# Optimization experiments

Measured on AMD Instinct MI355X. Metric: run time of the kernel, lower is better.

Reference implementation:

```python
import jax, jax.numpy as jnp
import numpy as np

T, H = 8192, 2048


def setup_inputs() -> dict:
    key = jax.random.key(0)
    k1, k2, k3 = jax.random.split(key, 3)
    x_sequence = jax.random.normal(k1, (T, H), dtype=jnp.float32)
    lamda = jax.random.normal(k2, (H,), dtype=jnp.float32) * 0.2
    B = jax.random.normal(k3, (H, H), dtype=jnp.float32) / np.sqrt(H).astype(np.float32)
    return {"x_sequence": x_sequence, "lamda": lamda, "B": B}


def reference(x_sequence, lamda, B):
    # Batched input projection: u_t = B @ x_t for all t -> one GEMM. [T, H]
    u = x_sequence @ B.T
    # Linear diagonal recurrence h_t = lamda * h_{t-1} + u_t with h_0 = 0,
    # solved with a log-depth associative scan over (a, b) pairs where
    # combine((a1,b1),(a2,b2)) = (a2*a1, a2*b1 + b2).
    a = jnp.broadcast_to(lamda, u.shape)  # [T, H]

    def combine(c1, c2):
        a1, b1 = c1
        a2, b2 = c2
        return (a2 * a1, a2 * b1 + b2)

    _, h = jax.lax.associative_scan(combine, (a, u))
    return h  # [T, H] stacked hidden states
```

## Files before the change

kernel.cpp:

```cpp
#include <hip/hip_runtime.h>
#include <hip/hip_bf16.h>


#define TDIM 8192
#define HDIM 2048
#define BM 256
#define BN 256
#define BK 32
#define NT (HDIM / BK)
#define ASLOT 8192
#define BSLOT 8192
#define LCH 64
#define GCH (TDIM / LCH)

#define XBF_BYTES (TDIM * HDIM * 2)
#define BBF_BYTES (HDIM * HDIM * 2)
#define E_BYTES   (GCH * HDIM * 4)
#define WS_NEED   ((size_t)XBF_BYTES + BBF_BYTES + E_BYTES)

typedef float f32x4 __attribute__((ext_vector_type(4)));
typedef short s16x4 __attribute__((ext_vector_type(4)));
typedef short s16x8 __attribute__((ext_vector_type(8)));

static __device__ __forceinline__ short f2bf(float f) {
  __bf16 b = (__bf16)f;
  return __builtin_bit_cast(short, b);
}

#define SB()   asm volatile("s_barrier" ::: "memory")
#define VMW(n) asm volatile("s_waitcnt vmcnt(" #n ")" ::: "memory")
#define GL(gp, lp)                                                            \
  __builtin_amdgcn_global_load_lds(                                           \
      (const __attribute__((address_space(1))) void*)(gp),                    \
      (__attribute__((address_space(3))) void*)(lp), 16, 0, 0)

__global__ void cvt_fast2(const float* __restrict__ X, const float* __restrict__ Bm,
                          short* __restrict__ Xb, short* __restrict__ Bb) {
  const int b = blockIdx.x;
  const float* s;
  short* d;
  int base;
  if (b < 4096) { s = X;  d = Xb; base = b * 1024; }
  else          { s = Bm; d = Bb; base = (b - 4096) * 1024; }
  const int t = threadIdx.x;
  f32x4 v0 = *(const f32x4*)(s + (size_t)(base +   0 + t) * 4);
  f32x4 v1 = *(const f32x4*)(s + (size_t)(base + 256 + t) * 4);
  f32x4 v2 = *(const f32x4*)(s + (size_t)(base + 512 + t) * 4);
  f32x4 v3 = *(const f32x4*)(s + (size_t)(base + 768 + t) * 4);
#define STORE1(v_, off_) do {                                                 \
    s16x4 o;                                                                  \
    o[0] = f2bf(v_[0]); o[1] = f2bf(v_[1]);                                   \
    o[2] = f2bf(v_[2]); o[3] = f2bf(v_[3]);                                   \
    *(s16x4*)(d + (size_t)(base + (off_) + t) * 4) = o;                       \
  } while (0)
  STORE1(v0, 0);
  STORE1(v1, 256);
  STORE1(v2, 512);
  STORE1(v3, 768);
#undef STORE1
}

__global__ __launch_bounds__(512, 2) void gemm8p2(
    const short* __restrict__ Xb, const short* __restrict__ Bb,
    float* __restrict__ U) {
  extern __shared__ __align__(16) short smem[];
  short* As = smem;
  short* Bs = smem + 4 * ASLOT;

  const int wg  = blockIdx.x;
  const int swz = (wg & 7) * 32 + (wg >> 3);
  const int tm = swz >> 3;
  const int tn = swz & 7;
  const int row0 = tm * BM, col0 = tn * BN;

  const int tid  = threadIdx.x;
  const int lane = tid & 63;
  const int wid  = tid >> 6;
  const int wr = (wid >> 2) * 128;
  const int wc = (wid & 3) * 64;
  const int r16 = lane & 15;
  const int ks8 = (lane >> 4) * 8;

  int offA[8], offB[4];
#pragma unroll
  for (int m = 0; m < 8; ++m) {
    const int r = wr + m * 16 + r16;
    offA[m] = r * BK + (ks8 ^ (((r >> 1) & 3) * 8));
  }
#pragma unroll
  for (int n = 0; n < 4; ++n) {
    const int r = wc + n * 16 + r16;
    offB[n] = r * BK + (ks8 ^ (((r >> 1) & 3) * 8));
  }

  const int srow = tid >> 2;
  const int sg   = (tid & 3) ^ ((tid >> 3) & 3);
  const short* gA0 = Xb + (size_t)(row0 + srow) * HDIM + sg * 8;
  const short* gA1 = gA0 + (size_t)128 * HDIM;
  const short* gB0 = Bb + (size_t)(col0 + srow) * HDIM + sg * 8;
  const short* gB1 = gB0 + (size_t)128 * HDIM;

  f32x4 acc[8][4] = {};

#pragma unroll
  for (int k = 0; k < 3; ++k) {
    GL(gA0 + k * BK, &As[k * ASLOT + tid * 8]);
    GL(gA1 + k * BK, &As[k * ASLOT + 4096 + tid * 8]);
    GL(gB0 + k * BK, &Bs[k * BSLOT + tid * 8]);
    GL(gB1 + k * BK, &Bs[k * BSLOT + 4096 + tid * 8]);
  }
  VMW(8);
  SB();

#define ITER(J_, ST_, VMA_, SBF_) do {                                        \
    const int sc_ = (J_) & 3;                                                 \
    const int si_ = ((J_) + 3) & 3;                                           \
    const int ko_ = ((J_) + 3) * BK;                                          \
    s16x8 af[4], bfv[4];                                                      \
    _Pragma("unroll") for (int m = 0; m < 4; ++m)                             \
      af[m] = *(const s16x8*)&As[sc_ * ASLOT + offA[m]];                      \
    _Pragma("unroll") for (int n = 0; n < 4; ++n)                             \
      bfv[n] = *(const s16x8*)&Bs[sc_ * BSLOT + offB[n]];                     \
    if (ST_) {                                                                \
      GL(gA0 + ko_, &As[si_ * ASLOT + tid * 8]);                              \
      GL(gA1 + ko_, &As[si_ * ASLOT + 4096 + tid * 8]);                       \
    }                                                                         \
    SB();                                                                     \
    __builtin_amdgcn_s_setprio(1);                                            \
    _Pragma("unroll") for (int m = 0; m < 4; ++m)                             \
      _Pragma("unroll") for (int n = 0; n < 4; ++n)                           \
        acc[m][n] = __builtin_amdgcn_mfma_f32_16x16x32_bf16(                  \
            af[m], bfv[n], acc[m][n], 0, 0, 0);                               \
    __builtin_amdgcn_s_setprio(0);                                            \
    SB();                                                                     \
    _Pragma("unroll") for (int m = 0; m < 4; ++m)                             \
      af[m] = *(const s16x8*)&As[sc_ * ASLOT + offA[4 + m]];                  \
    if (ST_) {                                                                \
      GL(gB0 + ko_, &Bs[si_ * BSLOT + tid * 8]);                              \
      GL(gB1 + ko_, &Bs[si_ * BSLOT + 4096 + tid * 8]);                       \
    }                                                                         \
    SB();                                                                     \
    __builtin_amdgcn_s_setprio(1);                                            \
    _Pragma("unroll") for (int m = 0; m < 4; ++m)                             \
      _Pragma("unroll") for (int n = 0; n < 4; ++n)                           \
        acc[4 + m][n] = __builtin_amdgcn_mfma_f32_16x16x32_bf16(              \
            af[m], bfv[n], acc[4 + m][n], 0, 0, 0);                           \
    __builtin_amdgcn_s_setprio(0);                                            \
    VMA_;                                                                     \
    SBF_;                                                                     \
  } while (0)

#pragma unroll 4
  for (int j = 0; j < NT - 4; ++j) ITER(j, true, VMW(8), SB());
  ITER(NT - 4, true,  VMW(8), SB());
  ITER(NT - 3, false, VMW(4), SB());
  ITER(NT - 2, false, VMW(0), SB());
  ITER(NT - 1, false, (void)0, (void)0);
#undef ITER

  const int crow = row0 + wr + ((lane >> 4) << 2);
  const int ccol = col0 + wc + r16;
#pragma unroll
  for (int m = 0; m < 8; ++m)
#pragma unroll
    for (int n = 0; n < 4; ++n)
#pragma unroll
      for (int j = 0; j < 4; ++j)
        U[(size_t)(crow + m * 16 + j) * HDIM + ccol + n * 16] = acc[m][n][j];
}

__global__ __launch_bounds__(256, 2) void gemm_f32_fb(
    const float* __restrict__ X, const float* __restrict__ Bm,
    float* __restrict__ U) {
#define LDK 40
#define FBM 128
#define FBK 32
#define FNT (HDIM / FBK)
  __shared__ __align__(16) short As[2][FBM * LDK];
  __shared__ __align__(16) short Bs[2][FBM * LDK];
  const int wg  = blockIdx.x;
  const int cpx = (TDIM / FBM) * (HDIM / FBM) / 8;
  const int swz = (wg & 7) * cpx + (wg >> 3);
  const int tm = swz >> 4;
  const int tn = swz & 15;
  const int row0 = tm * FBM, col0 = tn * FBM;
  const int tid  = threadIdx.x;
  const int lane = tid & 63;
  const int wid  = tid >> 6;
  const int wr = (wid >> 1) * 64;
  const int wc = (wid & 1) * 64;
  const int srow = tid >> 2;
  const int sk   = (tid & 3) << 3;
  const float* gA  = X  + (size_t)(row0 + srow) * HDIM + sk;
  const float* gA2 = gA + 64 * HDIM;
  const float* gB  = Bm + (size_t)(col0 + srow) * HDIM + sk;
  const float* gB2 = gB + 64 * HDIM;
  f32x4 a00, a01, a10, a11, b00, b01, b10, b11;
#define LOADREG(kt) do {                                                      \
    const float* p;                                                           \
    p = gA  + (kt) * FBK; a00 = *(const f32x4*)p; a01 = *(const f32x4*)(p+4); \
    p = gA2 + (kt) * FBK; a10 = *(const f32x4*)p; a11 = *(const f32x4*)(p+4); \
    p = gB  + (kt) * FBK; b00 = *(const f32x4*)p; b01 = *(const f32x4*)(p+4); \
    p = gB2 + (kt) * FBK; b10 = *(const f32x4*)p; b11 = *(const f32x4*)(p+4); \
  } while (0)
#define CVT8(v, lo, hi) do {                                                  \
    v[0] = f2bf(lo[0]); v[1] = f2bf(lo[1]); v[2] = f2bf(lo[2]);               \
    v[3] = f2bf(lo[3]); v[4] = f2bf(hi[0]); v[5] = f2bf(hi[1]);               \
    v[6] = f2bf(hi[2]); v[7] = f2bf(hi[3]);                                   \
  } while (0)
#define DSWRITE(buf) do {                                                     \
    s16x8 v;                                                                  \
    CVT8(v, a00, a01); *(s16x8*)&As[buf][srow * LDK + sk] = v;                \
    CVT8(v, a10, a11); *(s16x8*)&As[buf][(srow + 64) * LDK + sk] = v;         \
    CVT8(v, b00, b01); *(s16x8*)&Bs[buf][srow * LDK + sk] = v;                \
    CVT8(v, b10, b11); *(s16x8*)&Bs[buf][(srow + 64) * LDK + sk] = v;         \
  } while (0)
  f32x4 acc[4][4] = {};
#define COMPUTE(buf) do {                                                     \
    const int r16_ = lane & 15;                                               \
    const int ks_  = (lane >> 4) * 8;                                         \
    s16x8 af[4], bfr[4];                                                      \
    _Pragma("unroll") for (int m = 0; m < 4; ++m)                             \
      af[m] = *(const s16x8*)&As[buf][(wr + m * 16 + r16_) * LDK + ks_];      \
    _Pragma("unroll") for (int n = 0; n < 4; ++n)                             \
      bfr[n] = *(const s16x8*)&Bs[buf][(wc + n * 16 + r16_) * LDK + ks_];     \
    _Pragma("unroll") for (int m = 0; m < 4; ++m)                             \
      _Pragma("unroll") for (int n = 0; n < 4; ++n)                           \
        acc[m][n] = __builtin_amdgcn_mfma_f32_16x16x32_bf16(                  \
            af[m], bfr[n], acc[m][n], 0, 0, 0);                               \
  } while (0)
  LOADREG(0);
  DSWRITE(0);
  __syncthreads();
#pragma unroll 2
  for (int kt = 0; kt < FNT; ++kt) {
    const int cur = kt & 1;
    if (kt + 1 < FNT) LOADREG(kt + 1);
    COMPUTE(cur);
    if (kt + 1 < FNT) DSWRITE(cur ^ 1);
    __syncthreads();
  }
  const int crow = wr + ((lane >> 4) << 2);
  const int ccol = wc + (lane & 15);
#pragma unroll
  for (int m = 0; m < 4; ++m)
#pragma unroll
    for (int n = 0; n < 4; ++n)
#pragma unroll
      for (int j = 0; j < 4; ++j)
        U[(size_t)(row0 + crow + m * 16 + j) * HDIM + (col0 + ccol + n * 16)] =
            acc[m][n][j];
#undef LOADREG
#undef CVT8
#undef DSWRITE
#undef COMPUTE
#undef LDK
#undef FBM
#undef FBK
#undef FNT
}

__global__ void scan_pass1(const float* __restrict__ U,
                           const float* __restrict__ lam,
                           float* __restrict__ e) {
  const int c = (blockIdx.y * 256 + threadIdx.x) * 4;
  const int j = blockIdx.x;
  const f32x4 l4 = *(const f32x4*)&lam[c];
  f32x4 h = {0.f, 0.f, 0.f, 0.f};
  const float* up = U + (size_t)j * LCH * HDIM + c;
#pragma unroll 4
  for (int t = 0; t < LCH; ++t) {
    f32x4 u4 = *(const f32x4*)up;
    h = l4 * h + u4;
    up += HDIM;
  }
  *(f32x4*)&e[(size_t)j * HDIM + c] = h;
}

__global__ void scan_carry(float* __restrict__ e, const float* __restrict__ lam) {
  const int c = (blockIdx.x * 256 + threadIdx.x) * 4;
  const f32x4 l4 = *(const f32x4*)&lam[c];
  f32x4 p = l4;
#pragma unroll
  for (int i = 0; i < 6; ++i) p = p * p;
  f32x4 E = {0.f, 0.f, 0.f, 0.f};
  for (int j = 0; j < GCH; ++j) {
    f32x4 ej = *(const f32x4*)&e[(size_t)j * HDIM + c];
    *(f32x4*)&e[(size_t)j * HDIM + c] = E;
    E = p * E + ej;
  }
}

__global__ void scan_pass3(float* __restrict__ U, const float* __restrict__ lam,
                           const float* __restrict__ carry) {
  const int c = (blockIdx.y * 256 + threadIdx.x) * 4;
  const int j = blockIdx.x;
  const f32x4 l4 = *(const f32x4*)&lam[c];
  f32x4 h = *(const f32x4*)&carry[(size_t)j * HDIM + c];
  float* up = U + (size_t)j * LCH * HDIM + c;
#pragma unroll 4
  for (int t = 0; t < LCH; ++t) {
    f32x4 u4 = *(const f32x4*)up;
    h = l4 * h + u4;
    *(f32x4*)up = h;
    up += HDIM;
  }
}

extern "C" void kernel_launch(void* const* d_in, const int* in_sizes, int n_in,
                              void* d_out, int out_size, void* d_ws, size_t ws_size,
                              hipStream_t stream) {
  const float* X   = (const float*)d_in[0];
  const float* lam = (const float*)d_in[1];
  const float* Bm  = (const float*)d_in[2];
  float* U = (float*)d_out;

  if (ws_size >= WS_NEED) {
    short* Xb = (short*)d_ws;
    short* Bb = (short*)((char*)d_ws + XBF_BYTES);
    float* e  = (float*)((char*)d_ws + XBF_BYTES + BBF_BYTES);

    hipFuncSetAttribute((const void*)gemm8p2,
                        hipFuncAttributeMaxDynamicSharedMemorySize, 131072);

    cvt_fast2<<<dim3(5120), dim3(256), 0, stream>>>(X, Bm, Xb, Bb);
    gemm8p2<<<dim3((TDIM / BM) * (HDIM / BN)), dim3(512), 131072, stream>>>(
        Xb, Bb, U);
    scan_pass1<<<dim3(GCH, HDIM / 1024), dim3(256), 0, stream>>>(U, lam, e);
    scan_carry<<<dim3(HDIM / 1024), dim3(256), 0, stream>>>(e, lam);
    scan_pass3<<<dim3(GCH, HDIM / 1024), dim3(256), 0, stream>>>(U, lam, e);
  } else {
    float* e = (float*)d_ws;
    gemm_f32_fb<<<dim3((TDIM / 128) * (HDIM / 128)), dim3(256), 0, stream>>>(
        X, Bm, U);
    scan_pass1<<<dim3(GCH, HDIM / 1024), dim3(256), 0, stream>>>(U, lam, e);
    scan_carry<<<dim3(HDIM / 1024), dim3(256), 0, stream>>>(e, lam);
    scan_pass3<<<dim3(GCH, HDIM / 1024), dim3(256), 0, stream>>>(U, lam, e);
  }
}
```

Before: 128.8 us.

## Fuse X fp32-to-bf16 conversion into GEMM A-tile LDS read path

Drops the separate conversion pass over X. The GEMM now streams fp32 X tiles straight into LDS, using a new 4-byte XOR swizzle, and converts to bf16 when it reads the A fragments. The pipeline goes from 4 stages to 3 to fit the larger fp32 A tiles in LDS. This saves writing and rereading a 32 MB bf16 copy of X, but it doubles the global and LDS bytes for A and adds conversion ALU work inside the main loop.

```diff
diff --git a/kernel.cpp b/kernel.cpp
--- a/kernel.cpp
+++ b/kernel.cpp
@@ -8,15 +8,15 @@
 #define BN 256
 #define BK 32
 #define NT (HDIM / BK)
-#define ASLOT 8192
-#define BSLOT 8192
+#define AF 8192
+#define BS 8192
 #define LCH 64
 #define GCH (TDIM / LCH)
 
-#define XBF_BYTES (TDIM * HDIM * 2)
 #define BBF_BYTES (HDIM * HDIM * 2)
 #define E_BYTES   (GCH * HDIM * 4)
-#define WS_NEED   ((size_t)XBF_BYTES + BBF_BYTES + E_BYTES)
+#define WS_NEED   ((size_t)BBF_BYTES + E_BYTES)
+#define LDS_BYTES (3 * AF * 4 + 3 * BS * 2)
 
 typedef float f32x4 __attribute__((ext_vector_type(4)));
 typedef short s16x4 __attribute__((ext_vector_type(4)));
@@ -34,38 +34,30 @@
       (const __attribute__((address_space(1))) void*)(gp),                    \
       (__attribute__((address_space(3))) void*)(lp), 16, 0, 0)
 
-__global__ void cvt_fast2(const float* __restrict__ X, const float* __restrict__ Bm,
-                          short* __restrict__ Xb, short* __restrict__ Bb) {
+__global__ void cvt_B(const float* __restrict__ src, short* __restrict__ dst) {
   const int b = blockIdx.x;
-  const float* s;
-  short* d;
-  int base;
-  if (b < 4096) { s = X;  d = Xb; base = b * 1024; }
-  else          { s = Bm; d = Bb; base = (b - 4096) * 1024; }
+  const int base = b * 1024;
   const int t = threadIdx.x;
-  f32x4 v0 = *(const f32x4*)(s + (size_t)(base +   0 + t) * 4);
-  f32x4 v1 = *(const f32x4*)(s + (size_t)(base + 256 + t) * 4);
-  f32x4 v2 = *(const f32x4*)(s + (size_t)(base + 512 + t) * 4);
-  f32x4 v3 = *(const f32x4*)(s + (size_t)(base + 768 + t) * 4);
+  f32x4 v0 = *(const f32x4*)(src + (size_t)(base +   0 + t) * 4);
+  f32x4 v1 = *(const f32x4*)(src + (size_t)(base + 256 + t) * 4);
+  f32x4 v2 = *(const f32x4*)(src + (size_t)(base + 512 + t) * 4);
+  f32x4 v3 = *(const f32x4*)(src + (size_t)(base + 768 + t) * 4);
 #define STORE1(v_, off_) do {                                                 \
     s16x4 o;                                                                  \
     o[0] = f2bf(v_[0]); o[1] = f2bf(v_[1]);                                   \
     o[2] = f2bf(v_[2]); o[3] = f2bf(v_[3]);                                   \
-    *(s16x4*)(d + (size_t)(base + (off_) + t) * 4) = o;                       \
-  } while (0)
-  STORE1(v0, 0);
-  STORE1(v1, 256);
-  STORE1(v2, 512);
-  STORE1(v3, 768);
+    *(s16x4*)(dst + (size_t)(base + (off_) + t) * 4) = o;                     \
+  } while (0)
+  STORE1(v0, 0); STORE1(v1, 256); STORE1(v2, 512); STORE1(v3, 768);
 #undef STORE1
 }
 
-__global__ __launch_bounds__(512, 2) void gemm8p2(
-    const short* __restrict__ Xb, const short* __restrict__ Bb,
+__global__ __launch_bounds__(512, 2) void gemm_f32a(
+    const float* __restrict__ X, const short* __restrict__ Bb,
     float* __restrict__ U) {
-  extern __shared__ __align__(16) short smem[];
-  short* As = smem;
-  short* Bs = smem + 4 * ASLOT;
+  extern __shared__ __align__(16) char smemc[];
+  float* As = (float*)smemc;
+  short* Bs = (short*)(smemc + 3 * AF * 4);
 
   const int wg  = blockIdx.x;
   const int swz = (wg & 7) * 32 + (wg >> 3);
@@ -79,52 +71,56 @@
   const int wr = (wid >> 2) * 128;
   const int wc = (wid & 3) * 64;
   const int r16 = lane & 15;
-  const int ks8 = (lane >> 4) * 8;
+  const int g4  = lane >> 4;
+  const int ks8 = g4 * 8;
 
   int offA[8], offB[4];
 #pragma unroll
   for (int m = 0; m < 8; ++m) {
     const int r = wr + m * 16 + r16;
-    offA[m] = r * BK + (ks8 ^ (((r >> 1) & 3) * 8));
+    offA[m] = r * 32 + (((g4 * 2) ^ (r & 7)) << 2);
   }
 #pragma unroll
   for (int n = 0; n < 4; ++n) {
     const int r = wc + n * 16 + r16;
-    offB[n] = r * BK + (ks8 ^ (((r >> 1) & 3) * 8));
-  }
-
-  const int srow = tid >> 2;
-  const int sg   = (tid & 3) ^ ((tid >> 3) & 3);
-  const short* gA0 = Xb + (size_t)(row0 + srow) * HDIM + sg * 8;
-  const short* gA1 = gA0 + (size_t)128 * HDIM;
-  const short* gB0 = Bb + (size_t)(col0 + srow) * HDIM + sg * 8;
+    offB[n] = r * 32 + (ks8 ^ (((r >> 1) & 3) * 8));
+  }
+
+  const int sgl = (tid & 7) ^ ((tid >> 3) & 7);
+  const float* gAf = X + (size_t)(row0 + (tid >> 3)) * HDIM + sgl * 4;
+  const int srowB = tid >> 2;
+  const int sgB   = (tid & 3) ^ ((tid >> 3) & 3);
+  const short* gB0 = Bb + (size_t)(col0 + srowB) * HDIM + sgB * 8;
   const short* gB1 = gB0 + (size_t)128 * HDIM;
 
+#define STAGE_A(sl, t_) do {                                                  \
+    _Pragma("unroll") for (int c = 0; c < 4; ++c)                             \
+      GL(gAf + (size_t)c * 64 * HDIM + (t_) * BK,                             \
+         &As[(sl) * AF + (c * 512 + tid) * 4]);                               \
+  } while (0)
+
+#define STAGE_B(sl, t_) do {                                                  \
+    GL(gB0 + (t_) * BK, &Bs[(sl) * BS + tid * 8]);                            \
+    GL(gB1 + (t_) * BK, &Bs[(sl) * BS + 4096 + tid * 8]);                     \
+  } while (0)
+
+#define AFRAG(dst, sl_, m_) do {                                              \
+    f32x4 lo_ = *(const f32x4*)&As[(sl_) * AF + offA[m_]];                    \
+    f32x4 hi_ = *(const f32x4*)&As[(sl_) * AF + (offA[m_] ^ 4)];              \
+    dst[0] = f2bf(lo_[0]); dst[1] = f2bf(lo_[1]);                             \
+    dst[2] = f2bf(lo_[2]); dst[3] = f2bf(lo_[3]);                             \
+    dst[4] = f2bf(hi_[0]); dst[5] = f2bf(hi_[1]);                             \
+    dst[6] = f2bf(hi_[2]); dst[7] = f2bf(hi_[3]);                             \
+  } while (0)
+
   f32x4 acc[8][4] = {};
 
-#pragma unroll
-  for (int k = 0; k < 3; ++k) {
-    GL(gA0 + k * BK, &As[k * ASLOT + tid * 8]);
-    GL(gA1 + k * BK, &As[k * ASLOT + 4096 + tid * 8]);
-    GL(gB0 + k * BK, &Bs[k * BSLOT + tid * 8]);
-    GL(gB1 + k * BK, &Bs[k * BSLOT + 4096 + tid * 8]);
-  }
-  VMW(8);
-  SB();
-
-#define ITER(J_, ST_, VMA_, SBF_) do {                                        \
-    const int sc_ = (J_) & 3;                                                 \
-    const int si_ = ((J_) + 3) & 3;                                           \
-    const int ko_ = ((J_) + 3) * BK;                                          \
+#define ITER(SC_, SI_, T_, ST_, VMA_, SBF_) do {                              \
     s16x8 af[4], bfv[4];                                                      \
-    _Pragma("unroll") for (int m = 0; m < 4; ++m)                             \
-      af[m] = *(const s16x8*)&As[sc_ * ASLOT + offA[m]];                      \
+    _Pragma("unroll") for (int m = 0; m < 4; ++m) AFRAG(af[m], SC_, m);       \
     _Pragma("unroll") for (int n = 0; n < 4; ++n)                             \
-      bfv[n] = *(const s16x8*)&Bs[sc_ * BSLOT + offB[n]];                     \
-    if (ST_) {                                                                \
-      GL(gA0 + ko_, &As[si_ * ASLOT + tid * 8]);                              \
-      GL(gA1 + ko_, &As[si_ * ASLOT + 4096 + tid * 8]);                       \
-    }                                                                         \
+      bfv[n] = *(const s16x8*)&Bs[(SC_) * BS + offB[n]];                      \
+    if (ST_) STAGE_A(SI_, T_);                                                \
     SB();                                                                     \
     __builtin_amdgcn_s_setprio(1);                                            \
     _Pragma("unroll") for (int m = 0; m < 4; ++m)                             \
@@ -133,12 +129,8 @@
             af[m], bfv[n], acc[m][n], 0, 0, 0);                               \
     __builtin_amdgcn_s_setprio(0);                                            \
     SB();                                                                     \
-    _Pragma("unroll") for (int m = 0; m < 4; ++m)                             \
-      af[m] = *(const s16x8*)&As[sc_ * ASLOT + offA[4 + m]];                  \
-    if (ST_) {                                                                \
-      GL(gB0 + ko_, &Bs[si_ * BSLOT + tid * 8]);                              \
-      GL(gB1 + ko_, &Bs[si_ * BSLOT + 4096 + tid * 8]);                       \
-    }                                                                         \
+    _Pragma("unroll") for (int m = 0; m < 4; ++m) AFRAG(af[m], SC_, 4 + m);   \
+    if (ST_) STAGE_B(SI_, T_);                                                \
     SB();                                                                     \
     __builtin_amdgcn_s_setprio(1);                                            \
     _Pragma("unroll") for (int m = 0; m < 4; ++m)                             \
@@ -150,15 +142,27 @@
     SBF_;                                                                     \
   } while (0)
 
-#pragma unroll 4
-  for (int j = 0; j < NT - 4; ++j) ITER(j, true, VMW(8), SB());
-  ITER(NT - 4, true,  VMW(8), SB());
-  ITER(NT - 3, false, VMW(4), SB());
-  ITER(NT - 2, false, VMW(0), SB());
-  ITER(NT - 1, false, (void)0, (void)0);
+  STAGE_A(0, 0); STAGE_B(0, 0);
+  STAGE_A(1, 1); STAGE_B(1, 1);
+  VMW(6);
+  SB();
+
+#pragma unroll 1
+  for (int j = 0; j < 60; j += 3) {
+    ITER(0, 2, j + 2, true, VMW(6), SB());
+    ITER(1, 0, j + 3, true, VMW(6), SB());
+    ITER(2, 1, j + 4, true, VMW(6), SB());
+  }
+  ITER(0, 2, 62, true, VMW(6), SB());
+  ITER(1, 0, 63, true, VMW(6), SB());
+  ITER(2, 0, 0, false, VMW(0), SB());
+  ITER(0, 0, 0, false, (void)0, (void)0);
 #undef ITER
-
-  const int crow = row0 + wr + ((lane >> 4) << 2);
+#undef AFRAG
+#undef STAGE_A
+#undef STAGE_B
+
+  const int crow = row0 + wr + (g4 << 2);
   const int ccol = col0 + wc + r16;
 #pragma unroll
   for (int m = 0; m < 8; ++m)
@@ -316,16 +320,15 @@
   float* U = (float*)d_out;
 
   if (ws_size >= WS_NEED) {
-    short* Xb = (short*)d_ws;
-    short* Bb = (short*)((char*)d_ws + XBF_BYTES);
-    float* e  = (float*)((char*)d_ws + XBF_BYTES + BBF_BYTES);
-
-    hipFuncSetAttribute((const void*)gemm8p2,
-                        hipFuncAttributeMaxDynamicSharedMemorySize, 131072);
-
-    cvt_fast2<<<dim3(5120), dim3(256), 0, stream>>>(X, Bm, Xb, Bb);
-    gemm8p2<<<dim3((TDIM / BM) * (HDIM / BN)), dim3(512), 131072, stream>>>(
-        Xb, Bb, U);
+    short* Bb = (short*)d_ws;
+    float* e  = (float*)((char*)d_ws + BBF_BYTES);
+
+    hipFuncSetAttribute((const void*)gemm_f32a,
+                        hipFuncAttributeMaxDynamicSharedMemorySize, LDS_BYTES);
+
+    cvt_B<<<dim3(HDIM * HDIM / 4096), dim3(256), 0, stream>>>(Bm, Bb);
+    gemm_f32a<<<dim3((TDIM / BM) * (HDIM / BN)), dim3(512), LDS_BYTES, stream>>>(
+        X, Bb, U);
     scan_pass1<<<dim3(GCH, HDIM / 1024), dim3(256), 0, stream>>>(U, lam, e);
     scan_carry<<<dim3(HDIM / 1024), dim3(256), 0, stream>>>(e, lam);
     scan_pass3<<<dim3(GCH, HDIM / 1024), dim3(256), 0, stream>>>(U, lam, e);
```

Result: slower. 134.5 us (+4.4%).
